# Optimization experiments

Hardware: AMD Instinct MI355X
Metric: run time of the kernel (lower is better)

## Reference

```python
import jax, jax.numpy as jnp
import numpy as np

N_NODES = 65536
N_EDGES = 524288
N_GRAPHS = 512
G_NODES = 10000
NUM_DISEASES = 2000
IN_DIM = 128
HID = 256  # 2 * IN_DIM (z_emb concat feat)
D_FEAT = 512
C_FEAT = 512
MAX_Z = 4000


def setup_inputs() -> dict:
    key = jax.random.key(0)
    ks = jax.random.split(key, 20)
    rn = lambda k, shape: jax.random.normal(k, shape, dtype=jnp.float32) * 0.05
    return {
        "z": jax.random.randint(ks[0], (N_NODES,), 0, MAX_Z),
        "node_id": jnp.sort(jax.random.randint(ks[1], (N_NODES,), 0, G_NODES)),
        "src": jax.random.randint(ks[2], (N_EDGES,), 0, N_NODES),
        "dst": jax.random.randint(ks[3], (N_EDGES,), 0, N_NODES),
        "graph_ids": jnp.sort(jax.random.randint(ks[4], (N_NODES,), 0, N_GRAPHS)),
        "z_table": rn(ks[5], (MAX_Z, IN_DIM)),
        "d_feat_tab": rn(ks[6], (G_NODES, D_FEAT)),
        "c_feat_tab": rn(ks[7], (G_NODES, C_FEAT)),
        "Wd": rn(ks[8], (D_FEAT, IN_DIM)),
        "Wc": rn(ks[9], (C_FEAT, IN_DIM)),
        "gin_W1": rn(ks[10], (HID, HID)), "gin_b1": jnp.zeros((HID,), jnp.float32),
        "gin_W2": rn(ks[11], (HID, HID)), "gin_b2": jnp.zeros((HID,), jnp.float32),
        "sage_Wself": rn(ks[12], (HID, HID)),
        "sage_Wneigh": rn(ks[13], (HID, HID)),
        "sage_b": jnp.zeros((HID,), jnp.float32),
        "lin1_W": rn(ks[14], (HID, HID)), "lin1_b": jnp.zeros((HID,), jnp.float32),
        "lin2_W": rn(ks[15], (HID, 1)), "lin2_b": jnp.zeros((1,), jnp.float32),
    }


def reference(z, node_id, src, dst, graph_ids, z_table, d_feat_tab, c_feat_tab,
              Wd, Wc, gin_W1, gin_b1, gin_W2, gin_b2,
              sage_Wself, sage_Wneigh, sage_b, lin1_W, lin1_b, lin2_W, lin2_b):
    # --- input feature construction (Model.forward) ---
    z_emb = z_table[z]                               # [N, IN_DIM]
    d_proj = d_feat_tab[node_id] @ Wd                # d_fc (bias=False)
    c_proj = c_feat_tab[node_id] @ Wc                # c_fc (bias=False)
    disease = (node_id <= NUM_DISEASES)[:, None]
    # node_id is sorted -> masked concat order == node order
    feat = jnp.where(disease, d_proj, c_proj)        # [N, IN_DIM]
    x = jnp.concatenate([z_emb, feat], axis=1)       # [N, HID]
    # --- GINConv: sum aggregation, eps=0, mlp = Lin->ReLU->Lin ---
    agg = jax.ops.segment_sum(x[src], dst, num_segments=N_NODES)
    h = x + agg
    h = jax.nn.relu(h @ gin_W1 + gin_b1) @ gin_W2 + gin_b2
    # --- SAGEConv('mean'): fc_self(h) + fc_neigh(mean_neighbors) + bias ---
    deg = jax.ops.segment_sum(jnp.ones((N_EDGES,), h.dtype), dst, num_segments=N_NODES)
    mean_n = jax.ops.segment_sum(h[src], dst, num_segments=N_NODES) / jnp.maximum(deg, 1.0)[:, None]
    h = h @ sage_Wself + mean_n @ sage_Wneigh + sage_b
    # --- per-graph max pooling readout ---
    g = jax.ops.segment_max(h, graph_ids, num_segments=N_GRAPHS, indices_are_sorted=True)
    g = jnp.where(jnp.isfinite(g), g, 0.0)           # guard empty graphs
    # --- head: Linear -> ReLU -> (dropout p=0, eval) -> Linear ---
    h = jax.nn.relu(g @ lin1_W + lin1_b)
    return h @ lin2_W + lin2_b                       # [N_GRAPHS, 1]
```

## Files before the change

kernel.cpp:

```cpp
#include <hip/hip_runtime.h>
#include <hip/hip_bf16.h>

#define N_NODES     65536
#define N_EDGES     524288
#define N_GRAPHS    512
#define G_NODES_N   10000
#define NUM_DIS     2000
#define IN_DIM      128
#define HID         256
#define D_FEAT      512
#define MAX_Z       4000

typedef _Float16 half8 __attribute__((ext_vector_type(8)));
typedef float    f32x4 __attribute__((ext_vector_type(4)));

typedef __attribute__((address_space(1))) const void as1_void;
typedef __attribute__((address_space(3))) void       as3_void;

__global__ __launch_bounds__(256) void prep_kernel(
    const float* __restrict__ Ws, const float* __restrict__ Wn,
    const float* __restrict__ Wd, const float* __restrict__ Wc,
    const float* __restrict__ W1, const float* __restrict__ W2,
    const float* __restrict__ z_table,
    const int* __restrict__ z, const int* __restrict__ node_id,
    _Float16* __restrict__ WsT, _Float16* __restrict__ WnT,
    _Float16* __restrict__ WdT, _Float16* __restrict__ WcT,
    _Float16* __restrict__ W12P, _Float16* __restrict__ zt16,
    int2* __restrict__ zn2, int* __restrict__ cnt, int* __restrict__ flags)
{
    const int b = blockIdx.x;
    const int tid = threadIdx.x;
    if (b < 64) {
        __shared__ float tile[64][65];
        const float* W; _Float16* T; int K, N, k0, n0;
        if (b < 32) {
            const int mat = b >> 4, t = b & 15;
            K = HID; N = HID; k0 = (t >> 2) * 64; n0 = (t & 3) * 64;
            W = (mat == 0) ? Ws : Wn;
            T = (mat == 0) ? WsT : WnT;
        } else {
            const int bb = b - 32;
            const int mat = bb >> 4, t = bb & 15;
            K = D_FEAT; N = IN_DIM; k0 = (t >> 1) * 64; n0 = (t & 1) * 64;
            W = (mat == 0) ? Wd : Wc;
            T = (mat == 0) ? WdT : WcT;
        }
        const int tx = tid & 63, ty = tid >> 6;
        #pragma unroll
        for (int r = 0; r < 64; r += 4)
            tile[r + ty][tx] = W[(size_t)(k0 + r + ty) * N + n0 + tx];
        __syncthreads();
        #pragma unroll
        for (int c = 0; c < 64; c += 4)
            T[(size_t)(n0 + c + ty) * K + k0 + tx] = (_Float16)tile[tx][c + ty];
    } else if (b < 576) {
        const int bb = b - 64;
        const int mat = bb >> 8;
        const int k = bb & 255;
        const int n = tid;
        const float* W = mat ? W2 : W1;
        const float v = W[(size_t)k * HID + n];
        const size_t idx = (size_t)(mat * 8 + (k >> 5)) * 8192
                         + (size_t)((((k >> 3) & 3) * 256 + n) * 8 + (k & 7));
        W12P[idx] = (_Float16)v;
    } else if (b < 826) {
        const size_t base = ((size_t)(b - 576) * 256 + tid) * 8;
        const float4 f0 = *(const float4*)(z_table + base);
        const float4 f1 = *(const float4*)(z_table + base + 4);
        half8 h;
        h[0]=(_Float16)f0.x; h[1]=(_Float16)f0.y; h[2]=(_Float16)f0.z; h[3]=(_Float16)f0.w;
        h[4]=(_Float16)f1.x; h[5]=(_Float16)f1.y; h[6]=(_Float16)f1.z; h[7]=(_Float16)f1.w;
        *(half8*)(zt16 + base) = h;
    } else if (b < 890) {
        const int base = (b - 826) * 1024 + tid * 4;
        *(int4*)(cnt + base) = make_int4(0, 0, 0, 0);
        if (b == 826 && tid < 128) flags[tid] = 0;
    } else {
        const int i = (b - 890) * 256 + tid;
        zn2[i] = make_int2(z[i] << 8, node_id[i] << 8);
    }
}

__global__ __launch_bounds__(256) void proj_hist_kernel(
    const float* __restrict__ dtab, const float* __restrict__ ctab,
    const _Float16* __restrict__ WdT, const _Float16* __restrict__ WcT,
    _Float16* __restrict__ proj,
    const int* __restrict__ dst, int* __restrict__ cnt)
{
    const int blk = blockIdx.x;
    if (blk >= 79) {
        const int e = (blk - 79) * 256 + threadIdx.x;
        if (e < N_EDGES) atomicAdd(&cnt[dst[e]], 1);
        return;
    }
    __shared__ _Float16 Alds[128 * 40];
    __shared__ _Float16 Blds[128 * 40];
    const float* tab; const _Float16* WT; int base, M, bm;
    if (blk < 16) { tab = dtab; WT = WdT; base = 0;           M = NUM_DIS + 1;             bm = blk * 128; }
    else          { tab = ctab; WT = WcT; base = NUM_DIS + 1; M = G_NODES_N - NUM_DIS - 1; bm = (blk - 16) * 128; }
    const int tid  = threadIdx.x;
    const int wave = tid >> 6, lane = tid & 63;
    const int q    = lane >> 4, l16 = lane & 15;
    const int mbase = (wave & 1) * 64, nbase = (wave >> 1) * 64;
    const int r = tid >> 1, s = tid & 1;

    f32x4 acc[4][4] = {};

    for (int kc = 0; kc < 16; ++kc) {
        const int k0 = kc * 32;
        const int arow = min(bm + r, M - 1);
        const float* gA = tab + (size_t)(base + arow) * D_FEAT + k0 + s * 16;
        const _Float16* gB = WT + (size_t)r * D_FEAT + k0 + s * 16;
        const float4 f0 = ((const float4*)gA)[0];
        const float4 f1 = ((const float4*)gA)[1];
        const float4 f2 = ((const float4*)gA)[2];
        const float4 f3 = ((const float4*)gA)[3];
        const half8 hb0 = *(const half8*)gB;
        const half8 hb1 = *(const half8*)(gB + 8);
        half8 h0, h1;
        h0[0]=(_Float16)f0.x; h0[1]=(_Float16)f0.y; h0[2]=(_Float16)f0.z; h0[3]=(_Float16)f0.w;
        h0[4]=(_Float16)f1.x; h0[5]=(_Float16)f1.y; h0[6]=(_Float16)f1.z; h0[7]=(_Float16)f1.w;
        h1[0]=(_Float16)f2.x; h1[1]=(_Float16)f2.y; h1[2]=(_Float16)f2.z; h1[3]=(_Float16)f2.w;
        h1[4]=(_Float16)f3.x; h1[5]=(_Float16)f3.y; h1[6]=(_Float16)f3.z; h1[7]=(_Float16)f3.w;
        __syncthreads();
        *(half8*)&Alds[r * 40 + s * 16]     = h0;
        *(half8*)&Alds[r * 40 + s * 16 + 8] = h1;
        *(half8*)&Blds[r * 40 + s * 16]     = hb0;
        *(half8*)&Blds[r * 40 + s * 16 + 8] = hb1;
        __syncthreads();
        half8 a[4], b[4];
        #pragma unroll
        for (int i = 0; i < 4; ++i)
            a[i] = *(const half8*)&Alds[(mbase + i * 16 + l16) * 40 + q * 8];
        #pragma unroll
        for (int j = 0; j < 4; ++j)
            b[j] = *(const half8*)&Blds[(nbase + j * 16 + l16) * 40 + q * 8];
        #pragma unroll
        for (int i = 0; i < 4; ++i)
            #pragma unroll
            for (int j = 0; j < 4; ++j)
                acc[i][j] = __builtin_amdgcn_mfma_f32_16x16x32_f16(a[i], b[j], acc[i][j], 0, 0, 0);
    }

    #pragma unroll
    for (int j = 0; j < 4; ++j) {
        const int colg = nbase + j * 16 + l16;
        #pragma unroll
        for (int i = 0; i < 4; ++i) {
            #pragma unroll
            for (int rr = 0; rr < 4; ++rr) {
                const int row = bm + mbase + i * 16 + q * 4 + rr;
                if (row < M)
                    proj[(size_t)(base + row) * IN_DIM + colg] = (_Float16)acc[i][j][rr];
            }
        }
    }
}

__global__ __launch_bounds__(256) void scan_fused_kernel(
    const int* __restrict__ cnt, int* __restrict__ row_ptr,
    int* __restrict__ fill, int* __restrict__ flags)
{
    __shared__ int a[256], b[256];
    __shared__ int sums[64];
    __shared__ int segbase;
    const int t = threadIdx.x;
    const int blk = blockIdx.x;
    const int base = blk * 1024 + t * 4;
    const int4 c = *(const int4*)(cnt + base);
    const int s = c.x + c.y + c.z + c.w;
    a[t] = s;
    __syncthreads();
    int* in = a; int* out = b;
    for (int off = 1; off < 256; off <<= 1) {
        out[t] = in[t] + ((t >= off) ? in[t - off] : 0);
        __syncthreads();
        int* tmp = in; in = out; out = tmp;
    }
    if (t == 0) {
        atomicExch(&flags[64 + blk], in[255]);
        __threadfence();
        atomicAdd(&flags[0], 1);
        while (atomicAdd(&flags[0], 0) < 64) {}
    }
    __syncthreads();
    if (t < 64) sums[t] = atomicAdd(&flags[64 + t], 0);
    __syncthreads();
    if (t == 0) {
        int pfx = 0;
        for (int i = 0; i < blk; ++i) pfx += sums[i];
        segbase = pfx;
        if (blk == 63) {
            int tot = pfx;
            for (int i = blk; i < 64; ++i) tot += sums[i];
            row_ptr[N_NODES] = tot;
        }
    }
    __syncthreads();
    const int run = in[t] - s + segbase;
    int4 r;
    r.x = run; r.y = run + c.x; r.z = r.y + c.y; r.w = r.z + c.z;
    *(int4*)(row_ptr + base) = r;
    *(int4*)(fill + base) = r;
}

__global__ __launch_bounds__(256) void scatter_kernel(
    const int* __restrict__ src, const int* __restrict__ dst,
    const int2* __restrict__ zn2,
    int* __restrict__ fill, int* __restrict__ col, int2* __restrict__ colzn)
{
    const int e = blockIdx.x * 256 + threadIdx.x;
    if (e < N_EDGES) {
        const int s = src[e];
        const int pos = atomicAdd(&fill[dst[e]], 1);
        col[pos] = s;
        colzn[pos] = zn2[s];
    }
}

__global__ __launch_bounds__(512) void gin_fused_kernel(
    const int* __restrict__ row_ptr, const int2* __restrict__ colzn,
    const int2* __restrict__ zn2,
    const _Float16* __restrict__ zt16, const _Float16* __restrict__ proj,
    const _Float16* __restrict__ W12P,
    const float* __restrict__ b1, const float* __restrict__ b2,
    _Float16* __restrict__ H)
{
    __shared__ _Float16 Apanel[64 * 264];
    __shared__ _Float16 Blds[8192];

    const int bm   = blockIdx.x * 64;
    const int tid  = threadIdx.x;
    const int wave = tid >> 6, lane = tid & 63;
    const int q    = lane >> 4, l16 = lane & 15;
    const int wr   = wave >> 2;
    const int wc   = wave & 3;
    const int rbase = wr * 32;
    const int nbase = wc * 64;

    #pragma unroll
    for (int tt = 0; tt < 2; ++tt) {
        const int seg = (wave * 2 + tt) * 64 + lane;
        __builtin_amdgcn_global_load_lds((as1_void*)(W12P + seg * 8),
            (as3_void*)&Blds[(wave * 2 + tt) * 64 * 8], 16, 0, 0);
    }

    {
        const int p = tid & 7;
        const int r = tid >> 3;
        const int gr = bm + r;
        const int beg = row_ptr[gr], end = row_ptr[gr + 1];
        const char* ztb = (const char*)zt16 + p * 32;
        const char* prb = (const char*)proj + p * 32;
        float za[16], pa[16];
        {
            const int2 zn = zn2[gr];
            const half8* zp = (const half8*)(ztb + zn.x);
            const half8* pp = (const half8*)(prb + zn.y);
            const half8 z0 = zp[0], z1 = zp[1], p0 = pp[0], p1 = pp[1];
            #pragma unroll
            for (int i = 0; i < 8; ++i) {
                za[i] = (float)z0[i]; za[8 + i] = (float)z1[i];
                pa[i] = (float)p0[i]; pa[8 + i] = (float)p1[i];
            }
        }
        int e = beg;
        int2 iA, iB, iC, iD;
        if (e + 4 <= end) {
            iA = colzn[e]; iB = colzn[e + 1]; iC = colzn[e + 2]; iD = colzn[e + 3];
        }
        for (; e + 4 <= end; e += 4) {
            const half8* zpA = (const half8*)(ztb + iA.x);
            const half8* ppA = (const half8*)(prb + iA.y);
            const half8* zpB = (const half8*)(ztb + iB.x);
            const half8* ppB = (const half8*)(prb + iB.y);
            const half8* zpC = (const half8*)(ztb + iC.x);
            const half8* ppC = (const half8*)(prb + iC.y);
            const half8* zpD = (const half8*)(ztb + iD.x);
            const half8* ppD = (const half8*)(prb + iD.y);
            const half8 zA0 = zpA[0], zA1 = zpA[1], pA0 = ppA[0], pA1 = ppA[1];
            const half8 zB0 = zpB[0], zB1 = zpB[1], pB0 = ppB[0], pB1 = ppB[1];
            const half8 zC0 = zpC[0], zC1 = zpC[1], pC0 = ppC[0], pC1 = ppC[1];
            const half8 zD0 = zpD[0], zD1 = zpD[1], pD0 = ppD[0], pD1 = ppD[1];
            if (e + 8 <= end) {
                iA = colzn[e + 4]; iB = colzn[e + 5];
                iC = colzn[e + 6]; iD = colzn[e + 7];
            }
            #pragma unroll
            for (int i = 0; i < 8; ++i) {
                za[i]     += ((float)zA0[i] + (float)zB0[i]) + ((float)zC0[i] + (float)zD0[i]);
                za[8 + i] += ((float)zA1[i] + (float)zB1[i]) + ((float)zC1[i] + (float)zD1[i]);
                pa[i]     += ((float)pA0[i] + (float)pB0[i]) + ((float)pC0[i] + (float)pD0[i]);
                pa[8 + i] += ((float)pA1[i] + (float)pB1[i]) + ((float)pC1[i] + (float)pD1[i]);
            }
        }
        for (; e + 2 <= end; e += 2) {
            const int2 jA = colzn[e];
            const int2 jB = colzn[e + 1];
            const half8* zpA = (const half8*)(ztb + jA.x);
            const half8* ppA = (const half8*)(prb + jA.y);
            const half8* zpB = (const half8*)(ztb + jB.x);
            const half8* ppB = (const half8*)(prb + jB.y);
            const half8 zA0 = zpA[0], zA1 = zpA[1], pA0 = ppA[0], pA1 = ppA[1];
            const half8 zB0 = zpB[0], zB1 = zpB[1], pB0 = ppB[0], pB1 = ppB[1];
            #pragma unroll
            for (int i = 0; i < 8; ++i) {
                za[i]     += (float)zA0[i] + (float)zB0[i];
                za[8 + i] += (float)zA1[i] + (float)zB1[i];
                pa[i]     += (float)pA0[i] + (float)pB0[i];
                pa[8 + i] += (float)pA1[i] + (float)pB1[i];
            }
        }
        if (e < end) {
            const int2 jA = colzn[e];
            const half8* zp = (const half8*)(ztb + jA.x);
            const half8* pp = (const half8*)(prb + jA.y);
            const half8 z0 = zp[0], z1 = zp[1], p0 = pp[0], p1 = pp[1];
            #pragma unroll
            for (int i = 0; i < 8; ++i) {
                za[i] += (float)z0[i]; za[8 + i] += (float)z1[i];
                pa[i] += (float)p0[i]; pa[8 + i] += (float)p1[i];
            }
        }
        half8 oz0, oz1, op0, op1;
        #pragma unroll
        for (int i = 0; i < 8; ++i) {
            oz0[i] = (_Float16)za[i];     oz1[i] = (_Float16)za[8 + i];
            op0[i] = (_Float16)pa[i];     op1[i] = (_Float16)pa[8 + i];
        }
        *(half8*)&Apanel[r * 264 + p * 16]           = oz0;
        *(half8*)&Apanel[r * 264 + p * 16 + 8]       = oz1;
        *(half8*)&Apanel[r * 264 + 128 + p * 16]     = op0;
        *(half8*)&Apanel[r * 264 + 128 + p * 16 + 8] = op1;
    }
    __syncthreads();

    half8 pf0, pf1;
    auto pfetch = [&](int c) {
        const _Float16* s = W12P + (size_t)c * 8192 + (size_t)tid * 8;
        pf0 = *(const half8*)(s);
        pf1 = *(const half8*)(s + 4096);
    };
    pfetch(1);

    f32x4 acc[2][4] = {};
    for (int c = 0; c < 16; ++c) {
        const int kl = (c & 7) * 32;
        half8 a[2], b[4];
        #pragma unroll
        for (int i = 0; i < 2; ++i)
            a[i] = *(const half8*)&Apanel[(rbase + i * 16 + l16) * 264 + kl + q * 8];
        #pragma unroll
        for (int j = 0; j < 4; ++j)
            b[j] = *(const half8*)&Blds[(q * 256 + nbase + j * 16 + l16) * 8];
        #pragma unroll
        for (int i = 0; i < 2; ++i)
            #pragma unroll
            for (int j = 0; j < 4; ++j)
                acc[i][j] = __builtin_amdgcn_mfma_f32_16x16x32_f16(a[i], b[j], acc[i][j], 0, 0, 0);
        if (c == 15) break;
        __syncthreads();
        *(half8*)&Blds[tid * 8]         = pf0;
        *(half8*)&Blds[(tid + 512) * 8] = pf1;
        if (c == 7) {
            #pragma unroll
            for (int j = 0; j < 4; ++j) {
                const int colg = nbase + j * 16 + l16;
                const float bv = b1[colg];
                #pragma unroll
                for (int i = 0; i < 2; ++i)
                    #pragma unroll
                    for (int rr = 0; rr < 4; ++rr) {
                        const float v = fmaxf(acc[i][j][rr] + bv, 0.0f);
                        Apanel[(rbase + i * 16 + q * 4 + rr) * 264 + colg] = (_Float16)v;
                        acc[i][j][rr] = 0.0f;
                    }
            }
        }
        if (c < 14) pfetch(c + 2);
        __syncthreads();
    }

    #pragma unroll
    for (int j = 0; j < 4; ++j) {
        const int colg = nbase + j * 16 + l16;
        const float bv = b2[colg];
        #pragma unroll
        for (int i = 0; i < 2; ++i)
            #pragma unroll
            for (int rr = 0; rr < 4; ++rr) {
                const int rowg = bm + rbase + i * 16 + q * 4 + rr;
                H[(size_t)rowg * HID + colg] = (_Float16)(acc[i][j][rr] + bv);
            }
    }
}

__global__ __launch_bounds__(256) void csr_agg_kernel(
    const int* __restrict__ row_ptr, const int* __restrict__ col,
    const _Float16* __restrict__ F, _Float16* __restrict__ OUT)
{
    const int t = blockIdx.x * 256 + threadIdx.x;
    const int d = t >> 5;
    const int q = t & 31;
    const int beg = row_ptr[d];
    const int end = row_ptr[d + 1];
    float acc[8] = {0.f,0.f,0.f,0.f,0.f,0.f,0.f,0.f};
    int e = beg;
    for (; e + 8 <= end; e += 8) {
        const int s0 = col[e],     s1 = col[e + 1];
        const int s2 = col[e + 2], s3 = col[e + 3];
        const int s4 = col[e + 4], s5 = col[e + 5];
        const int s6 = col[e + 6], s7 = col[e + 7];
        const half8 v0 = *(const half8*)(F + (size_t)s0 * HID + q * 8);
        const half8 v1 = *(const half8*)(F + (size_t)s1 * HID + q * 8);
        const half8 v2 = *(const half8*)(F + (size_t)s2 * HID + q * 8);
        const half8 v3 = *(const half8*)(F + (size_t)s3 * HID + q * 8);
        const half8 v4 = *(const half8*)(F + (size_t)s4 * HID + q * 8);
        const half8 v5 = *(const half8*)(F + (size_t)s5 * HID + q * 8);
        const half8 v6 = *(const half8*)(F + (size_t)s6 * HID + q * 8);
        const half8 v7 = *(const half8*)(F + (size_t)s7 * HID + q * 8);
        #pragma unroll
        for (int i = 0; i < 8; ++i)
            acc[i] += (((float)v0[i] + (float)v1[i]) + ((float)v2[i] + (float)v3[i]))
                    + (((float)v4[i] + (float)v5[i]) + ((float)v6[i] + (float)v7[i]));
    }
    for (; e + 4 <= end; e += 4) {
        const int s0 = col[e],     s1 = col[e + 1];
        const int s2 = col[e + 2], s3 = col[e + 3];
        const half8 v0 = *(const half8*)(F + (size_t)s0 * HID + q * 8);
        const half8 v1 = *(const half8*)(F + (size_t)s1 * HID + q * 8);
        const half8 v2 = *(const half8*)(F + (size_t)s2 * HID + q * 8);
        const half8 v3 = *(const half8*)(F + (size_t)s3 * HID + q * 8);
        #pragma unroll
        for (int i = 0; i < 8; ++i)
            acc[i] += ((float)v0[i] + (float)v1[i]) + ((float)v2[i] + (float)v3[i]);
    }
    for (; e < end; ++e) {
        const half8 v0 = *(const half8*)(F + (size_t)col[e] * HID + q * 8);
        #pragma unroll
        for (int i = 0; i < 8; ++i) acc[i] += (float)v0[i];
    }
    const float rs = 1.0f / fmaxf((float)(end - beg), 1.0f);
    half8 o;
    #pragma unroll
    for (int i = 0; i < 8; ++i) o[i] = (_Float16)(acc[i] * rs);
    *(half8*)(OUT + (size_t)d * HID + q * 8) = o;
}

__global__ __launch_bounds__(256) void mfma_gemm_kernel(
    const _Float16* __restrict__ A1, const _Float16* __restrict__ A2,
    const _Float16* __restrict__ B1T, const _Float16* __restrict__ B2T,
    const float* __restrict__ bias, _Float16* __restrict__ Ch)
{
    __shared__ _Float16 Alds[128 * 32];
    __shared__ _Float16 Blds[128 * 32];
    const int bm   = blockIdx.x * 128;
    const int bn   = blockIdx.y * 128;
    const int tid  = threadIdx.x;
    const int wave = tid >> 6, lane = tid & 63;
    const int q    = lane >> 4, l16 = lane & 15;
    const int mbase = (wave & 1) * 64, nbase = (wave >> 1) * 64;

    const int i0 = wave * 128 + lane;
    const int i1 = i0 + 64;
    const int r0 = i0 >> 2, s0 = i0 & 3;
    const int r1 = i1 >> 2, s1 = i1 & 3;

    half8 pa0, pa1, pb0, pb1;
    auto pfetch = [&](int kc) {
        const int k0 = (kc & 7) * 32;
        const _Float16* Ab = (kc < 8) ? A1 : A2;
        const _Float16* Bb = (kc < 8) ? B1T : B2T;
        pa0 = *(const half8*)(Ab + (size_t)(bm + r0) * HID + k0 + s0 * 8);
        pa1 = *(const half8*)(Ab + (size_t)(bm + r1) * HID + k0 + s1 * 8);
        pb0 = *(const half8*)(Bb + (size_t)(bn + r0) * HID + k0 + s0 * 8);
        pb1 = *(const half8*)(Bb + (size_t)(bn + r1) * HID + k0 + s1 * 8);
    };
    pfetch(0);

    f32x4 acc[4][4] = {};

    for (int kc = 0; kc < 16; ++kc) {
        __syncthreads();
        *(half8*)&Alds[i0 * 8] = pa0;
        *(half8*)&Alds[i1 * 8] = pa1;
        *(half8*)&Blds[i0 * 8] = pb0;
        *(half8*)&Blds[i1 * 8] = pb1;
        if (kc < 15) pfetch(kc + 1);
        __syncthreads();
        half8 a[4], b[4];
        #pragma unroll
        for (int i = 0; i < 4; ++i)
            a[i] = *(const half8*)&Alds[(mbase + i * 16 + l16) * 32 + q * 8];
        #pragma unroll
        for (int j = 0; j < 4; ++j)
            b[j] = *(const half8*)&Blds[(nbase + j * 16 + l16) * 32 + q * 8];
        #pragma unroll
        for (int i = 0; i < 4; ++i)
            #pragma unroll
            for (int j = 0; j < 4; ++j)
                acc[i][j] = __builtin_amdgcn_mfma_f32_16x16x32_f16(a[i], b[j], acc[i][j], 0, 0, 0);
    }

    #pragma unroll
    for (int j = 0; j < 4; ++j) {
        const int colg = bn + nbase + j * 16 + l16;
        const float bv = bias[colg];
        #pragma unroll
        for (int i = 0; i < 4; ++i) {
            #pragma unroll
            for (int rr = 0; rr < 4; ++rr) {
                const int rowg = bm + mbase + i * 16 + q * 4 + rr;
                Ch[(size_t)rowg * HID + colg] = (_Float16)(acc[i][j][rr] + bv);
            }
        }
    }
}

__global__ __launch_bounds__(256) void pool_head_kernel(
    const _Float16* __restrict__ H2, const int* __restrict__ gid,
    const float* __restrict__ W1, const float* __restrict__ b1,
    const float* __restrict__ W2, const float* __restrict__ b2,
    float* __restrict__ out)
{
    const int g = blockIdx.x;
    const int tid = threadIdx.x;
    int lo = 0, hi = N_NODES;
    while (lo < hi) { const int mid = (lo + hi) >> 1; if (gid[mid] < g) lo = mid + 1; else hi = mid; }
    const int start = lo;
    hi = N_NODES;
    while (lo < hi) { const int mid = (lo + hi) >> 1; if (gid[mid] < g + 1) lo = mid + 1; else hi = mid; }
    const int end = lo;

    const int rowofs = tid >> 5;
    const int q = tid & 31;
    float m8[8];
    #pragma unroll
    for (int k = 0; k < 8; ++k) m8[k] = -INFINITY;
    for (int i = start + rowofs; i < end; i += 8) {
        const half8 v = *(const half8*)(H2 + (size_t)i * HID + q * 8);
        #pragma unroll
        for (int k = 0; k < 8; ++k) m8[k] = fmaxf(m8[k], (float)v[k]);
    }
    __shared__ float part[8][256];
    #pragma unroll
    for (int k = 0; k < 8; ++k) part[rowofs][q * 8 + k] = m8[k];
    __syncthreads();
    __shared__ float row[HID];
    __shared__ float red[HID];
    const int j = tid;
    float m = part[0][j];
    #pragma unroll
    for (int r = 1; r < 8; ++r) m = fmaxf(m, part[r][j]);
    row[j] = (m == -INFINITY) ? 0.0f : m;
    __syncthreads();
    float acc = b1[j];
    #pragma unroll 8
    for (int k = 0; k < HID; ++k)
        acc = fmaf(row[k], W1[k * HID + j], acc);
    acc = fmaxf(acc, 0.f);
    red[j] = acc * W2[j];
    __syncthreads();
    for (int s = 128; s > 0; s >>= 1) {
        if (j < s) red[j] += red[j + s];
        __syncthreads();
    }
    if (j == 0) out[g] = red[0] + b2[0];
}

extern "C" void kernel_launch(void* const* d_in, const int* in_sizes, int n_in,
                              void* d_out, int out_size, void* d_ws, size_t ws_size,
                              hipStream_t stream)
{
    const int*   z         = (const int*)d_in[0];
    const int*   node_id   = (const int*)d_in[1];
    const int*   src       = (const int*)d_in[2];
    const int*   dst       = (const int*)d_in[3];
    const int*   graph_ids = (const int*)d_in[4];
    const float* z_table   = (const float*)d_in[5];
    const float* d_feat    = (const float*)d_in[6];
    const float* c_feat    = (const float*)d_in[7];
    const float* Wd        = (const float*)d_in[8];
    const float* Wc        = (const float*)d_in[9];
    const float* gin_W1    = (const float*)d_in[10];
    const float* gin_b1    = (const float*)d_in[11];
    const float* gin_W2    = (const float*)d_in[12];
    const float* gin_b2    = (const float*)d_in[13];
    const float* sage_Wself  = (const float*)d_in[14];
    const float* sage_Wneigh = (const float*)d_in[15];
    const float* sage_b    = (const float*)d_in[16];
    const float* lin1_W    = (const float*)d_in[17];
    const float* lin1_b    = (const float*)d_in[18];
    const float* lin2_W    = (const float*)d_in[19];
    const float* lin2_b    = (const float*)d_in[20];
    float* out = (float*)d_out;

    const size_t NH = (size_t)N_NODES * HID;
    char* wsb = (char*)d_ws;
    _Float16* Hh   = (_Float16*)wsb;                     wsb += NH * 2;
    _Float16* AGGh = (_Float16*)wsb;                     wsb += NH * 2;
    _Float16* H2h  = (_Float16*)wsb;                     wsb += NH * 2;
    _Float16* projh= (_Float16*)wsb;                     wsb += (size_t)G_NODES_N * IN_DIM * 2;
    _Float16* W12P = (_Float16*)wsb;                     wsb += 16 * 8192 * 2;
    _Float16* WsT  = (_Float16*)wsb;                     wsb += HID * HID * 2;
    _Float16* WnT  = (_Float16*)wsb;                     wsb += HID * HID * 2;
    _Float16* WdT  = (_Float16*)wsb;                     wsb += D_FEAT * IN_DIM * 2;
    _Float16* WcT  = (_Float16*)wsb;                     wsb += D_FEAT * IN_DIM * 2;
    _Float16* zt16 = (_Float16*)wsb;                     wsb += (size_t)MAX_Z * IN_DIM * 2;
    int2* zn2      = (int2*)wsb;                         wsb += (size_t)N_NODES * 8;
    int2* colzn    = (int2*)wsb;                         wsb += (size_t)(N_EDGES + 8) * 8;
    int* row_ptr   = (int*)wsb;                          wsb += (N_NODES + 4) * 4;
    int* cnt       = (int*)wsb;                          wsb += N_NODES * 4;
    int* fill      = (int*)wsb;                          wsb += N_NODES * 4;
    int* col       = (int*)wsb;                          wsb += N_EDGES * 4;
    int* flags     = (int*)wsb;                          wsb += 128 * 4;

    prep_kernel<<<1146, 256, 0, stream>>>(
        sage_Wself, sage_Wneigh, Wd, Wc, gin_W1, gin_W2, z_table, z, node_id,
        WsT, WnT, WdT, WcT, W12P, zt16, zn2, cnt, flags);

    proj_hist_kernel<<<79 + N_EDGES / 256, 256, 0, stream>>>(
        d_feat, c_feat, WdT, WcT, projh, dst, cnt);

    scan_fused_kernel<<<64, 256, 0, stream>>>(cnt, row_ptr, fill, flags);
    scatter_kernel<<<N_EDGES / 256, 256, 0, stream>>>(src, dst, zn2, fill, col, colzn);

    gin_fused_kernel<<<N_NODES / 64, 512, 0, stream>>>(
        row_ptr, colzn, zn2, zt16, projh, W12P, gin_b1, gin_b2, Hh);

    csr_agg_kernel<<<(N_NODES * 32) / 256, 256, 0, stream>>>(row_ptr, col, Hh, AGGh);

    dim3 ggrid(N_NODES / 128, HID / 128);
    mfma_gemm_kernel<<<ggrid, 256, 0, stream>>>(Hh, AGGh, WsT, WnT, sage_b, H2h);

    pool_head_kernel<<<N_GRAPHS, 256, 0, stream>>>(
        H2h, graph_ids, lin1_W, lin1_b, lin2_W, lin2_b, out);
}
```

Measured before the change: 345.4 us.

## Bucket nodes by degree for load-balanced GIN and SAGE aggregation

```diff
diff --git a/kernel.cpp b/kernel.cpp
--- a/kernel.cpp
+++ b/kernel.cpp
@@ -159,17 +159,23 @@
 
 __global__ __launch_bounds__(256) void scan_fused_kernel(
     const int* __restrict__ cnt, int* __restrict__ row_ptr,
-    int* __restrict__ fill, int* __restrict__ flags)
+    int* __restrict__ fill, int* __restrict__ flags,
+    const int2* __restrict__ zn2, int2* __restrict__ pzn,
+    int2* __restrict__ prbe, int* __restrict__ pnode,
+    int* __restrict__ bhist)
 {
     __shared__ int a[256], b[256];
     __shared__ int sums[64];
     __shared__ int segbase;
+    __shared__ int hist[64];
+    __shared__ int pos[64];
     const int t = threadIdx.x;
     const int blk = blockIdx.x;
     const int base = blk * 1024 + t * 4;
     const int4 c = *(const int4*)(cnt + base);
     const int s = c.x + c.y + c.z + c.w;
     a[t] = s;
+    if (t < 64) hist[t] = 0;
     __syncthreads();
     int* in = a; int* out = b;
     for (int off = 1; off < 256; off <<= 1) {
@@ -202,6 +208,47 @@
     r.x = run; r.y = run + c.x; r.z = r.y + c.y; r.w = r.z + c.z;
     *(int4*)(row_ptr + base) = r;
     *(int4*)(fill + base) = r;
+
+    const int bk0 = min(c.x, 63), bk1 = min(c.y, 63);
+    const int bk2 = min(c.z, 63), bk3 = min(c.w, 63);
+    atomicAdd(&hist[bk0], 1); atomicAdd(&hist[bk1], 1);
+    atomicAdd(&hist[bk2], 1); atomicAdd(&hist[bk3], 1);
+    __syncthreads();
+    if (t < 64) bhist[blk * 64 + t] = hist[t];
+    __threadfence();
+    if (t == 0) {
+        atomicAdd(&flags[1], 1);
+        while (atomicAdd(&flags[1], 0) < 64) {}
+    }
+    __syncthreads();
+    if (t < 64) {
+        int pre = 0, tot = 0;
+        for (int i = 0; i < 64; ++i) {
+            const int v = atomicAdd(&bhist[i * 64 + t], 0);
+            if (i < blk) pre += v;
+            tot += v;
+        }
+        hist[t] = tot;
+        pos[t] = pre;
+    }
+    __syncthreads();
+    if (t == 0) {
+        int run2 = 0;
+        for (int i = 0; i < 64; ++i) { const int tt = hist[i]; hist[i] = run2; run2 += tt; }
+    }
+    __syncthreads();
+    if (t < 64) pos[t] = hist[t] + pos[t];
+    __syncthreads();
+    const int begs[4] = { r.x, r.y, r.z, r.w };
+    const int ends[4] = { r.y, r.z, r.w, r.w + c.w };
+    const int bks[4]  = { bk0, bk1, bk2, bk3 };
+    #pragma unroll
+    for (int k = 0; k < 4; ++k) {
+        const int p = atomicAdd(&pos[bks[k]], 1);
+        pzn[p]   = zn2[base + k];
+        prbe[p]  = make_int2(begs[k], ends[k]);
+        pnode[p] = base + k;
+    }
 }
 
 __global__ __launch_bounds__(256) void scatter_kernel(
@@ -218,9 +265,9 @@
     }
 }
 
-__global__ __launch_bounds__(512) void gin_fused_kernel(
-    const int* __restrict__ row_ptr, const int2* __restrict__ colzn,
-    const int2* __restrict__ zn2,
+__global__ __launch_bounds__(256) void gin_fused_kernel(
+    const int2* __restrict__ prbe, const int2* __restrict__ colzn,
+    const int2* __restrict__ pzn, const int* __restrict__ pnode,
     const _Float16* __restrict__ zt16, const _Float16* __restrict__ proj,
     const _Float16* __restrict__ W12P,
     const float* __restrict__ b1, const float* __restrict__ b2,
@@ -228,151 +275,160 @@
 {
     __shared__ _Float16 Apanel[64 * 264];
     __shared__ _Float16 Blds[8192];
+    __shared__ int prows[64];
 
     const int bm   = blockIdx.x * 64;
     const int tid  = threadIdx.x;
     const int wave = tid >> 6, lane = tid & 63;
     const int q    = lane >> 4, l16 = lane & 15;
-    const int wr   = wave >> 2;
-    const int wc   = wave & 3;
-    const int rbase = wr * 32;
-    const int nbase = wc * 64;
-
-    #pragma unroll
-    for (int tt = 0; tt < 2; ++tt) {
-        const int seg = (wave * 2 + tt) * 64 + lane;
+    const int nbase = wave * 64;
+    const int sb   = wave * 256 + lane;
+
+    if (tid < 64) prows[tid] = pnode[bm + tid];
+
+    #pragma unroll
+    for (int tt = 0; tt < 4; ++tt) {
+        const int seg = (wave * 4 + tt) * 64 + lane;
         __builtin_amdgcn_global_load_lds((as1_void*)(W12P + seg * 8),
-            (as3_void*)&Blds[(wave * 2 + tt) * 64 * 8], 16, 0, 0);
+            (as3_void*)&Blds[(wave * 4 + tt) * 64 * 8], 16, 0, 0);
     }
 
     {
         const int p = tid & 7;
-        const int r = tid >> 3;
-        const int gr = bm + r;
-        const int beg = row_ptr[gr], end = row_ptr[gr + 1];
         const char* ztb = (const char*)zt16 + p * 32;
         const char* prb = (const char*)proj + p * 32;
-        float za[16], pa[16];
-        {
-            const int2 zn = zn2[gr];
-            const half8* zp = (const half8*)(ztb + zn.x);
-            const half8* pp = (const half8*)(prb + zn.y);
-            const half8 z0 = zp[0], z1 = zp[1], p0 = pp[0], p1 = pp[1];
+        #pragma unroll 1
+        for (int pass = 0; pass < 2; ++pass) {
+            const int r  = (tid >> 3) + (pass << 5);
+            const int gr = bm + r;
+            const int2 be = prbe[gr];
+            const int beg = be.x, end = be.y;
+            float za[16], pa[16];
+            {
+                const int2 zn = pzn[gr];
+                const half8* zp = (const half8*)(ztb + zn.x);
+                const half8* pp = (const half8*)(prb + zn.y);
+                const half8 z0 = zp[0], z1 = zp[1], p0 = pp[0], p1 = pp[1];
+                #pragma unroll
+                for (int i = 0; i < 8; ++i) {
+                    za[i] = (float)z0[i]; za[8 + i] = (float)z1[i];
+                    pa[i] = (float)p0[i]; pa[8 + i] = (float)p1[i];
+                }
+            }
+            int e = beg;
+            int2 iA, iB, iC, iD;
+            if (e + 4 <= end) {
+                iA = colzn[e]; iB = colzn[e + 1]; iC = colzn[e + 2]; iD = colzn[e + 3];
+            }
+            for (; e + 4 <= end; e += 4) {
+                const half8* zpA = (const half8*)(ztb + iA.x);
+                const half8* ppA = (const half8*)(prb + iA.y);
+                const half8* zpB = (const half8*)(ztb + iB.x);
+                const half8* ppB = (const half8*)(prb + iB.y);
+                const half8* zpC = (const half8*)(ztb + iC.x);
+                const half8* ppC = (const half8*)(prb + iC.y);
+                const half8* zpD = (const half8*)(ztb + iD.x);
+                const half8* ppD = (const half8*)(prb + iD.y);
+                const half8 zA0 = zpA[0], zA1 = zpA[1], pA0 = ppA[0], pA1 = ppA[1];
+                const half8 zB0 = zpB[0], zB1 = zpB[1], pB0 = ppB[0], pB1 = ppB[1];
+                const half8 zC0 = zpC[0], zC1 = zpC[1], pC0 = ppC[0], pC1 = ppC[1];
+                const half8 zD0 = zpD[0], zD1 = zpD[1], pD0 = ppD[0], pD1 = ppD[1];
+                if (e + 8 <= end) {
+                    iA = colzn[e + 4]; iB = colzn[e + 5];
+                    iC = colzn[e + 6]; iD = colzn[e + 7];
+                }
+                #pragma unroll
+                for (int i = 0; i < 8; ++i) {
+                    za[i]     += ((float)zA0[i] + (float)zB0[i]) + ((float)zC0[i] + (float)zD0[i]);
+                    za[8 + i] += ((float)zA1[i] + (float)zB1[i]) + ((float)zC1[i] + (float)zD1[i]);
+                    pa[i]     += ((float)pA0[i] + (float)pB0[i]) + ((float)pC0[i] + (float)pD0[i]);
+                    pa[8 + i] += ((float)pA1[i] + (float)pB1[i]) + ((float)pC1[i] + (float)pD1[i]);
+                }
+            }
+            for (; e + 2 <= end; e += 2) {
+                const int2 jA = colzn[e];
+                const int2 jB = colzn[e + 1];
+                const half8* zpA = (const half8*)(ztb + jA.x);
+                const half8* ppA = (const half8*)(prb + jA.y);
+                const half8* zpB = (const half8*)(ztb + jB.x);
+                const half8* ppB = (const half8*)(prb + jB.y);
+                const half8 zA0 = zpA[0], zA1 = zpA[1], pA0 = ppA[0], pA1 = ppA[1];
+                const half8 zB0 = zpB[0], zB1 = zpB[1], pB0 = ppB[0], pB1 = ppB[1];
+                #pragma unroll
+                for (int i = 0; i < 8; ++i) {
+                    za[i]     += (float)zA0[i] + (float)zB0[i];
+                    za[8 + i] += (float)zA1[i] + (float)zB1[i];
+                    pa[i]     += (float)pA0[i] + (float)pB0[i];
+                    pa[8 + i] += (float)pA1[i] + (float)pB1[i];
+                }
+            }
+            if (e < end) {
+                const int2 jA = colzn[e];
+                const half8* zp = (const half8*)(ztb + jA.x);
+                const half8* pp = (const half8*)(prb + jA.y);
+                const half8 z0 = zp[0], z1 = zp[1], p0 = pp[0], p1 = pp[1];
+                #pragma unroll
+                for (int i = 0; i < 8; ++i) {
+                    za[i] += (float)z0[i]; za[8 + i] += (float)z1[i];
+                    pa[i] += (float)p0[i]; pa[8 + i] += (float)p1[i];
+                }
+            }
+            half8 oz0, oz1, op0, op1;
             #pragma unroll
             for (int i = 0; i < 8; ++i) {
-                za[i] = (float)z0[i]; za[8 + i] = (float)z1[i];
-                pa[i] = (float)p0[i]; pa[8 + i] = (float)p1[i];
-            }
+                oz0[i] = (_Float16)za[i];     oz1[i] = (_Float16)za[8 + i];
+                op0[i] = (_Float16)pa[i];     op1[i] = (_Float16)pa[8 + i];
+            }
+            *(half8*)&Apanel[r * 264 + p * 16]           = oz0;
+            *(half8*)&Apanel[r * 264 + p * 16 + 8]       = oz1;
+            *(half8*)&Apanel[r * 264 + 128 + p * 16]     = op0;
+            *(half8*)&Apanel[r * 264 + 128 + p * 16 + 8] = op1;
         }
-        int e = beg;
-        int2 iA, iB, iC, iD;
-        if (e + 4 <= end) {
-            iA = colzn[e]; iB = colzn[e + 1]; iC = colzn[e + 2]; iD = colzn[e + 3];
-        }
-        for (; e + 4 <= end; e += 4) {
-            const half8* zpA = (const half8*)(ztb + iA.x);
-            const half8* ppA = (const half8*)(prb + iA.y);
-            const half8* zpB = (const half8*)(ztb + iB.x);
-            const half8* ppB = (const half8*)(prb + iB.y);
-            const half8* zpC = (const half8*)(ztb + iC.x);
-            const half8* ppC = (const half8*)(prb + iC.y);
-            const half8* zpD = (const half8*)(ztb + iD.x);
-            const half8* ppD = (const half8*)(prb + iD.y);
-            const half8 zA0 = zpA[0], zA1 = zpA[1], pA0 = ppA[0], pA1 = ppA[1];
-            const half8 zB0 = zpB[0], zB1 = zpB[1], pB0 = ppB[0], pB1 = ppB[1];
-            const half8 zC0 = zpC[0], zC1 = zpC[1], pC0 = ppC[0], pC1 = ppC[1];
-            const half8 zD0 = zpD[0], zD1 = zpD[1], pD0 = ppD[0], pD1 = ppD[1];
-            if (e + 8 <= end) {
-                iA = colzn[e + 4]; iB = colzn[e + 5];
-                iC = colzn[e + 6]; iD = colzn[e + 7];
-            }
-            #pragma unroll
-            for (int i = 0; i < 8; ++i) {
-                za[i]     += ((float)zA0[i] + (float)zB0[i]) + ((float)zC0[i] + (float)zD0[i]);
-                za[8 + i] += ((float)zA1[i] + (float)zB1[i]) + ((float)zC1[i] + (float)zD1[i]);
-                pa[i]     += ((float)pA0[i] + (float)pB0[i]) + ((float)pC0[i] + (float)pD0[i]);
-                pa[8 + i] += ((float)pA1[i] + (float)pB1[i]) + ((float)pC1[i] + (float)pD1[i]);
-            }
-        }
-        for (; e + 2 <= end; e += 2) {
-            const int2 jA = colzn[e];
-            const int2 jB = colzn[e + 1];
-            const half8* zpA = (const half8*)(ztb + jA.x);
-            const half8* ppA = (const half8*)(prb + jA.y);
-            const half8* zpB = (const half8*)(ztb + jB.x);
-            const half8* ppB = (const half8*)(prb + jB.y);
-            const half8 zA0 = zpA[0], zA1 = zpA[1], pA0 = ppA[0], pA1 = ppA[1];
-            const half8 zB0 = zpB[0], zB1 = zpB[1], pB0 = ppB[0], pB1 = ppB[1];
-            #pragma unroll
-            for (int i = 0; i < 8; ++i) {
-                za[i]     += (float)zA0[i] + (float)zB0[i];
-                za[8 + i] += (float)zA1[i] + (float)zB1[i];
-                pa[i]     += (float)pA0[i] + (float)pB0[i];
-                pa[8 + i] += (float)pA1[i] + (float)pB1[i];
-            }
-        }
-        if (e < end) {
-            const int2 jA = colzn[e];
-            const half8* zp = (const half8*)(ztb + jA.x);
-            const half8* pp = (const half8*)(prb + jA.y);
-            const half8 z0 = zp[0], z1 = zp[1], p0 = pp[0], p1 = pp[1];
-            #pragma unroll
-            for (int i = 0; i < 8; ++i) {
-                za[i] += (float)z0[i]; za[8 + i] += (float)z1[i];
-                pa[i] += (float)p0[i]; pa[8 + i] += (float)p1[i];
-            }
-        }
-        half8 oz0, oz1, op0, op1;
-        #pragma unroll
-        for (int i = 0; i < 8; ++i) {
-            oz0[i] = (_Float16)za[i];     oz1[i] = (_Float16)za[8 + i];
-            op0[i] = (_Float16)pa[i];     op1[i] = (_Float16)pa[8 + i];
-        }
-        *(half8*)&Apanel[r * 264 + p * 16]           = oz0;
-        *(half8*)&Apanel[r * 264 + p * 16 + 8]       = oz1;
-        *(half8*)&Apanel[r * 264 + 128 + p * 16]     = op0;
-        *(half8*)&Apanel[r * 264 + 128 + p * 16 + 8] = op1;
-    }
-    __syncthreads();
-
-    half8 pf0, pf1;
+    }
+    __syncthreads();
+
+    half8 pf0, pf1, pf2, pf3;
     auto pfetch = [&](int c) {
-        const _Float16* s = W12P + (size_t)c * 8192 + (size_t)tid * 8;
+        const _Float16* s = W12P + (size_t)c * 8192 + (size_t)sb * 8;
         pf0 = *(const half8*)(s);
-        pf1 = *(const half8*)(s + 4096);
+        pf1 = *(const half8*)(s + 512);
+        pf2 = *(const half8*)(s + 1024);
+        pf3 = *(const half8*)(s + 1536);
     };
     pfetch(1);
 
-    f32x4 acc[2][4] = {};
+    f32x4 acc[4][4] = {};
     for (int c = 0; c < 16; ++c) {
         const int kl = (c & 7) * 32;
-        half8 a[2], b[4];
-        #pragma unroll
-        for (int i = 0; i < 2; ++i)
-            a[i] = *(const half8*)&Apanel[(rbase + i * 16 + l16) * 264 + kl + q * 8];
+        half8 a[4], b[4];
+        #pragma unroll
+        for (int i = 0; i < 4; ++i)
+            a[i] = *(const half8*)&Apanel[(i * 16 + l16) * 264 + kl + q * 8];
         #pragma unroll
         for (int j = 0; j < 4; ++j)
             b[j] = *(const half8*)&Blds[(q * 256 + nbase + j * 16 + l16) * 8];
         #pragma unroll
-        for (int i = 0; i < 2; ++i)
+        for (int i = 0; i < 4; ++i)
             #pragma unroll
             for (int j = 0; j < 4; ++j)
                 acc[i][j] = __builtin_amdgcn_mfma_f32_16x16x32_f16(a[i], b[j], acc[i][j], 0, 0, 0);
         if (c == 15) break;
         __syncthreads();
-        *(half8*)&Blds[tid * 8]         = pf0;
-        *(half8*)&Blds[(tid + 512) * 8] = pf1;
+        *(half8*)&Blds[sb * 8]         = pf0;
+        *(half8*)&Blds[(sb + 64) * 8]  = pf1;
+        *(half8*)&Blds[(sb + 128) * 8] = pf2;
+        *(half8*)&Blds[(sb + 192) * 8] = pf3;
         if (c == 7) {
             #pragma unroll
             for (int j = 0; j < 4; ++j) {
                 const int colg = nbase + j * 16 + l16;
                 const float bv = b1[colg];
                 #pragma unroll
-                for (int i = 0; i < 2; ++i)
+                for (int i = 0; i < 4; ++i)
                     #pragma unroll
                     for (int rr = 0; rr < 4; ++rr) {
                         const float v = fmaxf(acc[i][j][rr] + bv, 0.0f);
-                        Apanel[(rbase + i * 16 + q * 4 + rr) * 264 + colg] = (_Float16)v;
+                        Apanel[(i * 16 + q * 4 + rr) * 264 + colg] = (_Float16)v;
                         acc[i][j][rr] = 0.0f;
                     }
             }
@@ -386,24 +442,25 @@
         const int colg = nbase + j * 16 + l16;
         const float bv = b2[colg];
         #pragma unroll
-        for (int i = 0; i < 2; ++i)
+        for (int i = 0; i < 4; ++i)
             #pragma unroll
             for (int rr = 0; rr < 4; ++rr) {
-                const int rowg = bm + rbase + i * 16 + q * 4 + rr;
-                H[(size_t)rowg * HID + colg] = (_Float16)(acc[i][j][rr] + bv);
+                const int rowl = i * 16 + q * 4 + rr;
+                H[(size_t)prows[rowl] * HID + colg] = (_Float16)(acc[i][j][rr] + bv);
             }
     }
 }
 
 __global__ __launch_bounds__(256) void csr_agg_kernel(
-    const int* __restrict__ row_ptr, const int* __restrict__ col,
+    const int2* __restrict__ prbe, const int* __restrict__ pnode,
+    const int* __restrict__ col,
     const _Float16* __restrict__ F, _Float16* __restrict__ OUT)
 {
     const int t = blockIdx.x * 256 + threadIdx.x;
-    const int d = t >> 5;
+    const int i = t >> 5;
     const int q = t & 31;
-    const int beg = row_ptr[d];
-    const int end = row_ptr[d + 1];
+    const int2 be = prbe[i];
+    const int beg = be.x, end = be.y;
     float acc[8] = {0.f,0.f,0.f,0.f,0.f,0.f,0.f,0.f};
     int e = beg;
     for (; e + 8 <= end; e += 8) {
@@ -420,9 +477,9 @@
         const half8 v6 = *(const half8*)(F + (size_t)s6 * HID + q * 8);
         const half8 v7 = *(const half8*)(F + (size_t)s7 * HID + q * 8);
         #pragma unroll
-        for (int i = 0; i < 8; ++i)
-            acc[i] += (((float)v0[i] + (float)v1[i]) + ((float)v2[i] + (float)v3[i]))
-                    + (((float)v4[i] + (float)v5[i]) + ((float)v6[i] + (float)v7[i]));
+        for (int k = 0; k < 8; ++k)
+            acc[k] += (((float)v0[k] + (float)v1[k]) + ((float)v2[k] + (float)v3[k]))
+                    + (((float)v4[k] + (float)v5[k]) + ((float)v6[k] + (float)v7[k]));
     }
     for (; e + 4 <= end; e += 4) {
         const int s0 = col[e],     s1 = col[e + 1];
@@ -432,18 +489,19 @@
         const half8 v2 = *(const half8*)(F + (size_t)s2 * HID + q * 8);
         const half8 v3 = *(const half8*)(F + (size_t)s3 * HID + q * 8);
         #pragma unroll
-        for (int i = 0; i < 8; ++i)
-            acc[i] += ((float)v0[i] + (float)v1[i]) + ((float)v2[i] + (float)v3[i]);
+        for (int k = 0; k < 8; ++k)
+            acc[k] += ((float)v0[k] + (float)v1[k]) + ((float)v2[k] + (float)v3[k]);
     }
     for (; e < end; ++e) {
         const half8 v0 = *(const half8*)(F + (size_t)col[e] * HID + q * 8);
         #pragma unroll
-        for (int i = 0; i < 8; ++i) acc[i] += (float)v0[i];
+        for (int k = 0; k < 8; ++k) acc[k] += (float)v0[k];
     }
     const float rs = 1.0f / fmaxf((float)(end - beg), 1.0f);
     half8 o;
     #pragma unroll
-    for (int i = 0; i < 8; ++i) o[i] = (_Float16)(acc[i] * rs);
+    for (int k = 0; k < 8; ++k) o[k] = (_Float16)(acc[k] * rs);
+    const int d = pnode[i];
     *(half8*)(OUT + (size_t)d * HID + q * 8) = o;
 }
 
@@ -609,6 +667,10 @@
     _Float16* zt16 = (_Float16*)wsb;                     wsb += (size_t)MAX_Z * IN_DIM * 2;
     int2* zn2      = (int2*)wsb;                         wsb += (size_t)N_NODES * 8;
     int2* colzn    = (int2*)wsb;                         wsb += (size_t)(N_EDGES + 8) * 8;
+    int2* pzn      = (int2*)wsb;                         wsb += (size_t)N_NODES * 8;
+    int2* prbe     = (int2*)wsb;                         wsb += (size_t)N_NODES * 8;
+    int* pnode     = (int*)wsb;                          wsb += (size_t)N_NODES * 4;
+    int* bhist     = (int*)wsb;                          wsb += 64 * 64 * 4;
     int* row_ptr   = (int*)wsb;                          wsb += (N_NODES + 4) * 4;
     int* cnt       = (int*)wsb;                          wsb += N_NODES * 4;
     int* fill      = (int*)wsb;                          wsb += N_NODES * 4;
@@ -622,13 +684,15 @@
     proj_hist_kernel<<<79 + N_EDGES / 256, 256, 0, stream>>>(
         d_feat, c_feat, WdT, WcT, projh, dst, cnt);
 
-    scan_fused_kernel<<<64, 256, 0, stream>>>(cnt, row_ptr, fill, flags);
+    scan_fused_kernel<<<64, 256, 0, stream>>>(
+        cnt, row_ptr, fill, flags, zn2, pzn, prbe, pnode, bhist);
     scatter_kernel<<<N_EDGES / 256, 256, 0, stream>>>(src, dst, zn2, fill, col, colzn);
 
-    gin_fused_kernel<<<N_NODES / 64, 512, 0, stream>>>(
-        row_ptr, colzn, zn2, zt16, projh, W12P, gin_b1, gin_b2, Hh);
-
-    csr_agg_kernel<<<(N_NODES * 32) / 256, 256, 0, stream>>>(row_ptr, col, Hh, AGGh);
+    gin_fused_kernel<<<N_NODES / 64, 256, 0, stream>>>(
+        prbe, colzn, pzn, pnode, zt16, projh, W12P, gin_b1, gin_b2, Hh);
+
+    csr_agg_kernel<<<(N_NODES * 32) / 256, 256, 0, stream>>>(
+        prbe, pnode, col, Hh, AGGh);
 
     dim3 ggrid(N_NODES / 128, HID / 128);
     mfma_gemm_kernel<<<ggrid, 256, 0, stream>>>(Hh, AGGh, WsT, WnT, sage_b, H2h);
```

New measurement: 348.6 us. No clear change (+0.9%).
